# Performance work log

Measured on AMD Instinct MI355X. Metric: run time of the kernel, lower is better.

Reference implementation:

```python
import jax, jax.numpy as jnp
import numpy as np

SPARSITY = 0.1  # fraction k of weights kept (matches init sparsity)


def _subnet(scores, k):
    # Faithful to GetSubnet.forward: sort flattened scores ascending,
    # zero the bottom (1-k)*n entries, set the top k*n entries to 1.
    n = scores.size
    j = int((1.0 - k) * n)  # static under jit
    idx = jnp.argsort(scores.ravel())  # ascending, like torch .sort()
    flat = jnp.zeros((n,), scores.dtype).at[idx[j:]].set(1.0)
    return flat.reshape(scores.shape)


def setup_inputs() -> dict:
    key = jax.random.key(0)
    k1, k2 = jax.random.split(key)
    down_mask = jax.random.normal(k1, (8192, 2048), dtype=jnp.float32)
    up_mask = jax.random.normal(k2, (2048, 8192), dtype=jnp.float32)
    return {"down_mask": down_mask, "up_mask": up_mask}


def reference(down_mask, up_mask):
    # AdapterSubnet.forward: binary top-k masks of |down_mask| and |up_mask|
    return (_subnet(jnp.abs(down_mask), SPARSITY),
            _subnet(jnp.abs(up_mask), SPARSITY))
```

## Files before the change

kernel.cpp:

```cpp
#include <hip/hip_runtime.h>

using u32 = unsigned int;

#define H1_BINS 4096
#define H2_BINS 2048
#define H3_BINS 256
#define H1_OFF  0
#define H2_OFF  (H1_OFF + 2 * H1_BINS)
#define H3_OFF  (H2_OFF + 2 * H2_BINS)
#define SEL_OFF (H3_OFF + 2 * H3_BINS)
#define SEL_WORDS 8
#define EQ_OFF  (SEL_OFF + 2 * SEL_WORDS)
#define EQ_CAP  4096
#define ZERO_WORDS EQ_OFF

__device__ __forceinline__ u32 absbits(u32 x) { return x & 0x7FFFFFFFu; }

__global__ void k_hist1(const float* __restrict__ in0, const float* __restrict__ in1,
                        int n0, int n1, u32* __restrict__ ws) {
    __shared__ u32 h[H1_BINS];
    const int m = blockIdx.y;
    const u32* in = (const u32*)(m ? in1 : in0);
    const int n = m ? n1 : n0;
    const int n4 = n >> 2;
    for (int i = threadIdx.x; i < H1_BINS; i += blockDim.x) h[i] = 0;
    __syncthreads();
    const uint4* v = (const uint4*)in;
    const int stride = gridDim.x * blockDim.x;
    for (int i = blockIdx.x * blockDim.x + threadIdx.x; i < n4; i += stride) {
        uint4 x = v[i];
        atomicAdd(&h[absbits(x.x) >> 19], 1u);
        atomicAdd(&h[absbits(x.y) >> 19], 1u);
        atomicAdd(&h[absbits(x.z) >> 19], 1u);
        atomicAdd(&h[absbits(x.w) >> 19], 1u);
    }
    if (blockIdx.x == 0 && (int)threadIdx.x < (n & 3)) {
        u32 u = absbits(in[n4 * 4 + threadIdx.x]);
        atomicAdd(&h[u >> 19], 1u);
    }
    __syncthreads();
    u32* g = ws + H1_OFF + m * H1_BINS;
    for (int i = threadIdx.x; i < H1_BINS; i += blockDim.x)
        if (h[i]) atomicAdd(&g[i], h[i]);
}

__global__ void k_hist2(const float* __restrict__ in0, const float* __restrict__ in1,
                        int n0, int n1, u32* __restrict__ ws) {
    __shared__ u32 h[H2_BINS];
    const int m = blockIdx.y;
    const u32* in = (const u32*)(m ? in1 : in0);
    const int n = m ? n1 : n0;
    const int n4 = n >> 2;
    const u32 p1 = ws[SEL_OFF + m * SEL_WORDS + 0];
    for (int i = threadIdx.x; i < H2_BINS; i += blockDim.x) h[i] = 0;
    __syncthreads();
    const uint4* v = (const uint4*)in;
    const int stride = gridDim.x * blockDim.x;
    for (int i = blockIdx.x * blockDim.x + threadIdx.x; i < n4; i += stride) {
        uint4 x = v[i];
        u32 a;
        a = absbits(x.x); if ((a >> 19) == p1) atomicAdd(&h[(a >> 8) & 0x7FFu], 1u);
        a = absbits(x.y); if ((a >> 19) == p1) atomicAdd(&h[(a >> 8) & 0x7FFu], 1u);
        a = absbits(x.z); if ((a >> 19) == p1) atomicAdd(&h[(a >> 8) & 0x7FFu], 1u);
        a = absbits(x.w); if ((a >> 19) == p1) atomicAdd(&h[(a >> 8) & 0x7FFu], 1u);
    }
    if (blockIdx.x == 0 && (int)threadIdx.x < (n & 3)) {
        u32 a = absbits(in[n4 * 4 + threadIdx.x]);
        if ((a >> 19) == p1) atomicAdd(&h[(a >> 8) & 0x7FFu], 1u);
    }
    __syncthreads();
    u32* g = ws + H2_OFF + m * H2_BINS;
    for (int i = threadIdx.x; i < H2_BINS; i += blockDim.x)
        if (h[i]) atomicAdd(&g[i], h[i]);
}

__global__ void k_hist3(const float* __restrict__ in0, const float* __restrict__ in1,
                        int n0, int n1, u32* __restrict__ ws) {
    __shared__ u32 h[H3_BINS];
    const int m = blockIdx.y;
    const u32* in = (const u32*)(m ? in1 : in0);
    const int n = m ? n1 : n0;
    const int n4 = n >> 2;
    const u32* sel = ws + SEL_OFF + m * SEL_WORDS;
    const u32 pre20 = (sel[0] << 11) | sel[1];
    for (int i = threadIdx.x; i < H3_BINS; i += blockDim.x) h[i] = 0;
    __syncthreads();
    const uint4* v = (const uint4*)in;
    const int stride = gridDim.x * blockDim.x;
    for (int i = blockIdx.x * blockDim.x + threadIdx.x; i < n4; i += stride) {
        uint4 x = v[i];
        u32 a;
        a = absbits(x.x); if ((a >> 8) == pre20) atomicAdd(&h[a & 0xFFu], 1u);
        a = absbits(x.y); if ((a >> 8) == pre20) atomicAdd(&h[a & 0xFFu], 1u);
        a = absbits(x.z); if ((a >> 8) == pre20) atomicAdd(&h[a & 0xFFu], 1u);
        a = absbits(x.w); if ((a >> 8) == pre20) atomicAdd(&h[a & 0xFFu], 1u);
    }
    if (blockIdx.x == 0 && (int)threadIdx.x < (n & 3)) {
        u32 a = absbits(in[n4 * 4 + threadIdx.x]);
        if ((a >> 8) == pre20) atomicAdd(&h[a & 0xFFu], 1u);
    }
    __syncthreads();
    u32* g = ws + H3_OFF + m * H3_BINS;
    for (int i = threadIdx.x; i < H3_BINS; i += blockDim.x)
        if (h[i]) atomicAdd(&g[i], h[i]);
}

__global__ void k_select(u32* __restrict__ ws, int pass, int K0, int K1) {
    __shared__ u32 sh[256];
    const int m = blockIdx.x;
    u32* sel = ws + SEL_OFF + m * SEL_WORDS;
    const u32* hist;
    int bins;
    if (pass == 0)      { hist = ws + H1_OFF + m * H1_BINS; bins = H1_BINS; }
    else if (pass == 1) { hist = ws + H2_OFF + m * H2_BINS; bins = H2_BINS; }
    else                { hist = ws + H3_OFF + m * H3_BINS; bins = H3_BINS; }
    const u32 K = (u32)(m ? K1 : K0);
    u32 Gprev = 0;
    if (pass == 1) Gprev = sel[2];
    else if (pass == 2) Gprev = sel[5];
    const u32 Krem = K - Gprev;

    const int tid = threadIdx.x;
    const int C = bins / 256;
    const int base = tid * C;
    u32 s = 0;
    for (int i = 0; i < C; i++) s += hist[base + i];
    sh[tid] = s;
    __syncthreads();
    if (tid == 0) {
        u32 run = 0;
        for (int i = 255; i >= 0; i--) { u32 x = sh[i]; sh[i] = run; run += x; }
    }
    __syncthreads();
    u32 running = sh[tid];
    for (int bin = base + C - 1; bin >= base; bin--) {
        u32 c = hist[bin];
        if (running < Krem && running + c >= Krem) {
            if (pass == 0)      { sel[0] = (u32)bin; sel[2] = running; }
            else if (pass == 1) { sel[1] = (u32)bin; sel[5] = Gprev + running; }
            else {
                sel[3] = (sel[0] << 19) | (sel[1] << 8) | (u32)bin;
                sel[4] = Krem - running;
            }
        }
        running += c;
    }
}

__global__ void k_mask(const float* __restrict__ in0, const float* __restrict__ in1,
                       float* __restrict__ out0, float* __restrict__ out1,
                       int n0, int n1, u32* __restrict__ ws) {
    const int m = blockIdx.y;
    const u32* in = (const u32*)(m ? in1 : in0);
    float* out = m ? out1 : out0;
    const int n = m ? n1 : n0;
    const int n4 = n >> 2;
    u32* sel = ws + SEL_OFF + m * SEL_WORDS;
    const u32 t = sel[3];
    u32* eq = ws + EQ_OFF + m * EQ_CAP;
    const uint4* v = (const uint4*)in;
    float4* o = (float4*)out;
    const int stride = gridDim.x * blockDim.x;
    for (int i = blockIdx.x * blockDim.x + threadIdx.x; i < n4; i += stride) {
        uint4 x = v[i];
        u32 a0 = absbits(x.x), a1 = absbits(x.y), a2 = absbits(x.z), a3 = absbits(x.w);
        float4 r;
        r.x = (a0 > t) ? 1.0f : 0.0f;
        r.y = (a1 > t) ? 1.0f : 0.0f;
        r.z = (a2 > t) ? 1.0f : 0.0f;
        r.w = (a3 > t) ? 1.0f : 0.0f;
        o[i] = r;
        if (a0 == t) { u32 p = atomicAdd(&sel[6], 1u); if (p < EQ_CAP) eq[p] = (u32)(4 * i + 0); }
        if (a1 == t) { u32 p = atomicAdd(&sel[6], 1u); if (p < EQ_CAP) eq[p] = (u32)(4 * i + 1); }
        if (a2 == t) { u32 p = atomicAdd(&sel[6], 1u); if (p < EQ_CAP) eq[p] = (u32)(4 * i + 2); }
        if (a3 == t) { u32 p = atomicAdd(&sel[6], 1u); if (p < EQ_CAP) eq[p] = (u32)(4 * i + 3); }
    }
    if (blockIdx.x == 0 && (int)threadIdx.x < (n & 3)) {
        int idx = n4 * 4 + threadIdx.x;
        u32 a = absbits(in[idx]);
        out[idx] = (a > t) ? 1.0f : 0.0f;
        if (a == t) { u32 p = atomicAdd(&sel[6], 1u); if (p < EQ_CAP) eq[p] = (u32)idx; }
    }
}

__global__ void k_tie(float* __restrict__ out0, float* __restrict__ out1, u32* __restrict__ ws) {
    const int m = blockIdx.x;
    float* out = m ? out1 : out0;
    u32* sel = ws + SEL_OFF + m * SEL_WORDS;
    u32 E = sel[6]; if (E > EQ_CAP) E = EQ_CAP;
    const u32 R = sel[4];
    const u32* eq = ws + EQ_OFF + m * EQ_CAP;
    for (u32 e = threadIdx.x; e < E; e += blockDim.x) {
        u32 idx = eq[e];
        u32 cnt = 0;
        for (u32 e2 = 0; e2 < E; e2++) cnt += (eq[e2] > idx) ? 1u : 0u;
        if (cnt < R) out[idx] = 1.0f;
    }
}

extern "C" void kernel_launch(void* const* d_in, const int* in_sizes, int n_in,
                              void* d_out, int out_size, void* d_ws, size_t ws_size,
                              hipStream_t stream) {
    const float* in0 = (const float*)d_in[0];
    const float* in1 = (const float*)d_in[1];
    const int n0 = in_sizes[0];
    const int n1 = in_sizes[1];
    float* out0 = (float*)d_out;
    float* out1 = out0 + n0;
    u32* ws = (u32*)d_ws;

    const double k = 0.1;
    const int j0 = (int)((1.0 - k) * (double)n0);
    const int j1 = (int)((1.0 - k) * (double)n1);
    const int K0 = n0 - j0;
    const int K1 = n1 - j1;

    hipMemsetAsync(ws, 0, ZERO_WORDS * sizeof(u32), stream);

    dim3 hgrid(1024, 2);
    k_hist1<<<hgrid, 256, 0, stream>>>(in0, in1, n0, n1, ws);
    k_select<<<2, 256, 0, stream>>>(ws, 0, K0, K1);
    k_hist2<<<hgrid, 256, 0, stream>>>(in0, in1, n0, n1, ws);
    k_select<<<2, 256, 0, stream>>>(ws, 1, K0, K1);
    k_hist3<<<hgrid, 256, 0, stream>>>(in0, in1, n0, n1, ws);
    k_select<<<2, 256, 0, stream>>>(ws, 2, K0, K1);
    k_mask<<<dim3(1024, 2), 256, 0, stream>>>(in0, in1, out0, out1, n0, n1, ws);
    k_tie<<<2, 256, 0, stream>>>(out0, out1, ws);
}
```

Measured before the change: 335.0 us.

## Compact boundary-bucket candidates and fold select into last-block histogram kernels

```diff
diff --git a/kernel.cpp b/kernel.cpp
--- a/kernel.cpp
+++ b/kernel.cpp
@@ -1,6 +1,7 @@
 #include <hip/hip_runtime.h>
 
 using u32 = unsigned int;
+using u64 = unsigned long long;
 
 #define H1_BINS 4096
 #define H2_BINS 2048
@@ -9,155 +10,129 @@
 #define H2_OFF  (H1_OFF + 2 * H1_BINS)
 #define H3_OFF  (H2_OFF + 2 * H2_BINS)
 #define SEL_OFF (H3_OFF + 2 * H3_BINS)
-#define SEL_WORDS 8
-#define EQ_OFF  (SEL_OFF + 2 * SEL_WORDS)
-#define EQ_CAP  4096
-#define ZERO_WORDS EQ_OFF
+#define SEL_WORDS 16
+#define CTR_OFF  (SEL_OFF + 2 * SEL_WORDS)
+#define GCNT_OFF (CTR_OFF + 8)
+#define ECNT_OFF (GCNT_OFF + 2)
+#define ZERO_WORDS (ECNT_OFF + 2)
+#define EQ_OFF   12848
+#define EQ_CAP   4096
+#define CAND_OFF (EQ_OFF + 2 * EQ_CAP)
+#define GCAP     (1u << 21)
+#define SCAP     2048
 
 __device__ __forceinline__ u32 absbits(u32 x) { return x & 0x7FFFFFFFu; }
+__device__ __forceinline__ u32 aload(u32* p)  { return atomicAdd(p, 0u); }
+
+template<int BINS>
+__device__ void block_select(u32* hist, u32 Krem, u32* selBin, u32* selAbove) {
+    __shared__ u32 sh[256];
+    constexpr int C = BINS / 256;
+    u32 loc[C];
+    const int tid = threadIdx.x;
+    const int base = tid * C;
+    u32 s = 0;
+    for (int i = 0; i < C; i++) { loc[i] = aload(&hist[base + i]); s += loc[i]; }
+    sh[tid] = s;
+    __syncthreads();
+    if (tid == 0) {
+        u32 run = 0;
+        for (int i = 255; i >= 0; i--) { u32 x = sh[i]; sh[i] = run; run += x; }
+    }
+    __syncthreads();
+    u32 running = sh[tid];
+    for (int b = C - 1; b >= 0; b--) {
+        u32 c = loc[b];
+        if (running < Krem && running + c >= Krem) { *selBin = (u32)(base + b); *selAbove = running; }
+        running += c;
+    }
+}
 
 __global__ void k_hist1(const float* __restrict__ in0, const float* __restrict__ in1,
-                        int n0, int n1, u32* __restrict__ ws) {
-    __shared__ u32 h[H1_BINS];
+                        int n0, int n1, u32* __restrict__ ws, int K0, int K1) {
     const int m = blockIdx.y;
     const u32* in = (const u32*)(m ? in1 : in0);
     const int n = m ? n1 : n0;
     const int n4 = n >> 2;
-    for (int i = threadIdx.x; i < H1_BINS; i += blockDim.x) h[i] = 0;
-    __syncthreads();
+    u32* g = ws + H1_OFF + m * H1_BINS;
+    __shared__ u32 h[2][H1_BINS];
+    for (int i = threadIdx.x; i < H1_BINS; i += blockDim.x) { h[0][i] = 0; h[1][i] = 0; }
+    __syncthreads();
+    u32* hp = h[threadIdx.x >> 7];
     const uint4* v = (const uint4*)in;
     const int stride = gridDim.x * blockDim.x;
     for (int i = blockIdx.x * blockDim.x + threadIdx.x; i < n4; i += stride) {
         uint4 x = v[i];
-        atomicAdd(&h[absbits(x.x) >> 19], 1u);
-        atomicAdd(&h[absbits(x.y) >> 19], 1u);
-        atomicAdd(&h[absbits(x.z) >> 19], 1u);
-        atomicAdd(&h[absbits(x.w) >> 19], 1u);
-    }
-    if (blockIdx.x == 0 && (int)threadIdx.x < (n & 3)) {
-        u32 u = absbits(in[n4 * 4 + threadIdx.x]);
-        atomicAdd(&h[u >> 19], 1u);
-    }
-    __syncthreads();
-    u32* g = ws + H1_OFF + m * H1_BINS;
-    for (int i = threadIdx.x; i < H1_BINS; i += blockDim.x)
-        if (h[i]) atomicAdd(&g[i], h[i]);
-}
-
-__global__ void k_hist2(const float* __restrict__ in0, const float* __restrict__ in1,
-                        int n0, int n1, u32* __restrict__ ws) {
-    __shared__ u32 h[H2_BINS];
-    const int m = blockIdx.y;
-    const u32* in = (const u32*)(m ? in1 : in0);
-    const int n = m ? n1 : n0;
-    const int n4 = n >> 2;
-    const u32 p1 = ws[SEL_OFF + m * SEL_WORDS + 0];
-    for (int i = threadIdx.x; i < H2_BINS; i += blockDim.x) h[i] = 0;
-    __syncthreads();
-    const uint4* v = (const uint4*)in;
-    const int stride = gridDim.x * blockDim.x;
-    for (int i = blockIdx.x * blockDim.x + threadIdx.x; i < n4; i += stride) {
-        uint4 x = v[i];
-        u32 a;
-        a = absbits(x.x); if ((a >> 19) == p1) atomicAdd(&h[(a >> 8) & 0x7FFu], 1u);
-        a = absbits(x.y); if ((a >> 19) == p1) atomicAdd(&h[(a >> 8) & 0x7FFu], 1u);
-        a = absbits(x.z); if ((a >> 19) == p1) atomicAdd(&h[(a >> 8) & 0x7FFu], 1u);
-        a = absbits(x.w); if ((a >> 19) == p1) atomicAdd(&h[(a >> 8) & 0x7FFu], 1u);
-    }
-    if (blockIdx.x == 0 && (int)threadIdx.x < (n & 3)) {
-        u32 a = absbits(in[n4 * 4 + threadIdx.x]);
-        if ((a >> 19) == p1) atomicAdd(&h[(a >> 8) & 0x7FFu], 1u);
-    }
-    __syncthreads();
-    u32* g = ws + H2_OFF + m * H2_BINS;
-    for (int i = threadIdx.x; i < H2_BINS; i += blockDim.x)
-        if (h[i]) atomicAdd(&g[i], h[i]);
-}
-
-__global__ void k_hist3(const float* __restrict__ in0, const float* __restrict__ in1,
-                        int n0, int n1, u32* __restrict__ ws) {
-    __shared__ u32 h[H3_BINS];
-    const int m = blockIdx.y;
-    const u32* in = (const u32*)(m ? in1 : in0);
-    const int n = m ? n1 : n0;
-    const int n4 = n >> 2;
-    const u32* sel = ws + SEL_OFF + m * SEL_WORDS;
-    const u32 pre20 = (sel[0] << 11) | sel[1];
-    for (int i = threadIdx.x; i < H3_BINS; i += blockDim.x) h[i] = 0;
-    __syncthreads();
-    const uint4* v = (const uint4*)in;
-    const int stride = gridDim.x * blockDim.x;
-    for (int i = blockIdx.x * blockDim.x + threadIdx.x; i < n4; i += stride) {
-        uint4 x = v[i];
-        u32 a;
-        a = absbits(x.x); if ((a >> 8) == pre20) atomicAdd(&h[a & 0xFFu], 1u);
-        a = absbits(x.y); if ((a >> 8) == pre20) atomicAdd(&h[a & 0xFFu], 1u);
-        a = absbits(x.z); if ((a >> 8) == pre20) atomicAdd(&h[a & 0xFFu], 1u);
-        a = absbits(x.w); if ((a >> 8) == pre20) atomicAdd(&h[a & 0xFFu], 1u);
-    }
-    if (blockIdx.x == 0 && (int)threadIdx.x < (n & 3)) {
-        u32 a = absbits(in[n4 * 4 + threadIdx.x]);
-        if ((a >> 8) == pre20) atomicAdd(&h[a & 0xFFu], 1u);
-    }
-    __syncthreads();
-    u32* g = ws + H3_OFF + m * H3_BINS;
-    for (int i = threadIdx.x; i < H3_BINS; i += blockDim.x)
-        if (h[i]) atomicAdd(&g[i], h[i]);
-}
-
-__global__ void k_select(u32* __restrict__ ws, int pass, int K0, int K1) {
-    __shared__ u32 sh[256];
-    const int m = blockIdx.x;
-    u32* sel = ws + SEL_OFF + m * SEL_WORDS;
-    const u32* hist;
-    int bins;
-    if (pass == 0)      { hist = ws + H1_OFF + m * H1_BINS; bins = H1_BINS; }
-    else if (pass == 1) { hist = ws + H2_OFF + m * H2_BINS; bins = H2_BINS; }
-    else                { hist = ws + H3_OFF + m * H3_BINS; bins = H3_BINS; }
-    const u32 K = (u32)(m ? K1 : K0);
-    u32 Gprev = 0;
-    if (pass == 1) Gprev = sel[2];
-    else if (pass == 2) Gprev = sel[5];
-    const u32 Krem = K - Gprev;
-
-    const int tid = threadIdx.x;
-    const int C = bins / 256;
-    const int base = tid * C;
-    u32 s = 0;
-    for (int i = 0; i < C; i++) s += hist[base + i];
-    sh[tid] = s;
-    __syncthreads();
-    if (tid == 0) {
-        u32 run = 0;
-        for (int i = 255; i >= 0; i--) { u32 x = sh[i]; sh[i] = run; run += x; }
-    }
-    __syncthreads();
-    u32 running = sh[tid];
-    for (int bin = base + C - 1; bin >= base; bin--) {
-        u32 c = hist[bin];
-        if (running < Krem && running + c >= Krem) {
-            if (pass == 0)      { sel[0] = (u32)bin; sel[2] = running; }
-            else if (pass == 1) { sel[1] = (u32)bin; sel[5] = Gprev + running; }
-            else {
-                sel[3] = (sel[0] << 19) | (sel[1] << 8) | (u32)bin;
-                sel[4] = Krem - running;
-            }
-        }
-        running += c;
-    }
-}
-
-__global__ void k_mask(const float* __restrict__ in0, const float* __restrict__ in1,
-                       float* __restrict__ out0, float* __restrict__ out1,
-                       int n0, int n1, u32* __restrict__ ws) {
+        atomicAdd(&hp[absbits(x.x) >> 19], 1u);
+        atomicAdd(&hp[absbits(x.y) >> 19], 1u);
+        atomicAdd(&hp[absbits(x.z) >> 19], 1u);
+        atomicAdd(&hp[absbits(x.w) >> 19], 1u);
+    }
+    if (blockIdx.x == 0 && (int)threadIdx.x < (n & 3))
+        atomicAdd(&hp[absbits(in[n4 * 4 + threadIdx.x]) >> 19], 1u);
+    __syncthreads();
+    for (int i = threadIdx.x; i < H1_BINS; i += blockDim.x) {
+        u32 t = h[0][i] + h[1][i];
+        if (t) atomicAdd(&g[i], t);
+    }
+    __syncthreads();
+    __shared__ bool last;
+    if (threadIdx.x == 0) {
+        __threadfence();
+        last = (atomicAdd(&ws[CTR_OFF + m], 1u) == gridDim.x - 1);
+    }
+    __syncthreads();
+    if (last) {
+        __shared__ u32 tb, ta;
+        const u32 K = (u32)(m ? K1 : K0);
+        block_select<H1_BINS>(g, K, &tb, &ta);
+        __syncthreads();
+        if (threadIdx.x == 0) {
+            u32* sel = ws + SEL_OFF + m * SEL_WORDS;
+            sel[0] = tb;
+            sel[2] = ta;
+        }
+    }
+}
+
+__global__ void k_mask_compact(const float* __restrict__ in0, const float* __restrict__ in1,
+                               float* __restrict__ out0, float* __restrict__ out1,
+                               int n0, int n1, u32* __restrict__ ws) {
     const int m = blockIdx.y;
     const u32* in = (const u32*)(m ? in1 : in0);
     float* out = m ? out1 : out0;
     const int n = m ? n1 : n0;
     const int n4 = n >> 2;
-    u32* sel = ws + SEL_OFF + m * SEL_WORDS;
-    const u32 t = sel[3];
-    u32* eq = ws + EQ_OFF + m * EQ_CAP;
+    const u32 p1 = ws[SEL_OFF + m * SEL_WORDS + 0];
+    u32* gcnt = &ws[GCNT_OFF + m];
+    uint2* cand = (uint2*)(ws + CAND_OFF) + (size_t)m * GCAP;
+
+    __shared__ u32 scnt;
+    __shared__ u32 gbase;
+    __shared__ uint2 stage[SCAP];
+    if (threadIdx.x == 0) scnt = 0;
+    __syncthreads();
+
+    const u32 lane = threadIdx.x & 63u;
+    const u64 lmask = (1ull << lane) - 1ull;
+
+    auto handle = [&](u32 a, u32 idx) {
+        bool pred = ((a >> 19) == p1);
+        u64 mk = __ballot(pred);
+        if (mk) {
+            u32 cnt = (u32)__popcll(mk);
+            int leader = __ffsll((unsigned long long)mk) - 1;
+            u32 base = 0;
+            if ((int)lane == leader) base = atomicAdd(&scnt, cnt);
+            base = __shfl(base, leader);
+            if (pred) {
+                u32 pos = base + (u32)__popcll(mk & lmask);
+                if (pos < SCAP) stage[pos] = make_uint2(a, idx);
+                else { u32 gp = atomicAdd(gcnt, 1u); if (gp < GCAP) cand[gp] = make_uint2(a, idx); }
+            }
+        }
+    };
+
     const uint4* v = (const uint4*)in;
     float4* o = (float4*)out;
     const int stride = gridDim.x * blockDim.x;
@@ -165,36 +140,144 @@
         uint4 x = v[i];
         u32 a0 = absbits(x.x), a1 = absbits(x.y), a2 = absbits(x.z), a3 = absbits(x.w);
         float4 r;
-        r.x = (a0 > t) ? 1.0f : 0.0f;
-        r.y = (a1 > t) ? 1.0f : 0.0f;
-        r.z = (a2 > t) ? 1.0f : 0.0f;
-        r.w = (a3 > t) ? 1.0f : 0.0f;
+        r.x = ((a0 >> 19) > p1) ? 1.0f : 0.0f;
+        r.y = ((a1 >> 19) > p1) ? 1.0f : 0.0f;
+        r.z = ((a2 >> 19) > p1) ? 1.0f : 0.0f;
+        r.w = ((a3 >> 19) > p1) ? 1.0f : 0.0f;
         o[i] = r;
-        if (a0 == t) { u32 p = atomicAdd(&sel[6], 1u); if (p < EQ_CAP) eq[p] = (u32)(4 * i + 0); }
-        if (a1 == t) { u32 p = atomicAdd(&sel[6], 1u); if (p < EQ_CAP) eq[p] = (u32)(4 * i + 1); }
-        if (a2 == t) { u32 p = atomicAdd(&sel[6], 1u); if (p < EQ_CAP) eq[p] = (u32)(4 * i + 2); }
-        if (a3 == t) { u32 p = atomicAdd(&sel[6], 1u); if (p < EQ_CAP) eq[p] = (u32)(4 * i + 3); }
+        handle(a0, (u32)(4 * i + 0));
+        handle(a1, (u32)(4 * i + 1));
+        handle(a2, (u32)(4 * i + 2));
+        handle(a3, (u32)(4 * i + 3));
     }
     if (blockIdx.x == 0 && (int)threadIdx.x < (n & 3)) {
         int idx = n4 * 4 + threadIdx.x;
         u32 a = absbits(in[idx]);
-        out[idx] = (a > t) ? 1.0f : 0.0f;
-        if (a == t) { u32 p = atomicAdd(&sel[6], 1u); if (p < EQ_CAP) eq[p] = (u32)idx; }
-    }
-}
-
-__global__ void k_tie(float* __restrict__ out0, float* __restrict__ out1, u32* __restrict__ ws) {
-    const int m = blockIdx.x;
+        out[idx] = ((a >> 19) > p1) ? 1.0f : 0.0f;
+        handle(a, (u32)idx);
+    }
+    __syncthreads();
+    if (threadIdx.x == 0) {
+        u32 c = scnt < SCAP ? scnt : SCAP;
+        gbase = atomicAdd(gcnt, c);
+    }
+    __syncthreads();
+    u32 c = scnt < SCAP ? scnt : SCAP;
+    for (u32 j = threadIdx.x; j < c; j += blockDim.x) {
+        u32 p = gbase + j;
+        if (p < GCAP) cand[p] = stage[j];
+    }
+}
+
+__global__ void k_cand_hist2(u32* __restrict__ ws, int K0, int K1) {
+    const int m = blockIdx.y;
+    u32 cnt0 = ws[GCNT_OFF + m];
+    const u32 cnt = cnt0 < GCAP ? cnt0 : GCAP;
+    const uint2* cand = (const uint2*)(ws + CAND_OFF) + (size_t)m * GCAP;
+    u32* g = ws + H2_OFF + m * H2_BINS;
+    __shared__ u32 h[H2_BINS];
+    for (int i = threadIdx.x; i < H2_BINS; i += blockDim.x) h[i] = 0;
+    __syncthreads();
+    const u32 stride = gridDim.x * blockDim.x;
+    for (u32 i = blockIdx.x * blockDim.x + threadIdx.x; i < cnt; i += stride)
+        atomicAdd(&h[(cand[i].x >> 8) & 0x7FFu], 1u);
+    __syncthreads();
+    for (int i = threadIdx.x; i < H2_BINS; i += blockDim.x)
+        if (h[i]) atomicAdd(&g[i], h[i]);
+    __syncthreads();
+    __shared__ bool last;
+    if (threadIdx.x == 0) {
+        __threadfence();
+        last = (atomicAdd(&ws[CTR_OFF + 2 + m], 1u) == gridDim.x - 1);
+    }
+    __syncthreads();
+    if (last) {
+        u32* sel = ws + SEL_OFF + m * SEL_WORDS;
+        const u32 K = (u32)(m ? K1 : K0);
+        const u32 G1 = sel[2];
+        __shared__ u32 tb, ta;
+        block_select<H2_BINS>(g, K - G1, &tb, &ta);
+        __syncthreads();
+        if (threadIdx.x == 0) { sel[1] = tb; sel[5] = G1 + ta; }
+    }
+}
+
+__global__ void k_cand_hist3(u32* __restrict__ ws, int K0, int K1) {
+    const int m = blockIdx.y;
+    u32 cnt0 = ws[GCNT_OFF + m];
+    const u32 cnt = cnt0 < GCAP ? cnt0 : GCAP;
+    const uint2* cand = (const uint2*)(ws + CAND_OFF) + (size_t)m * GCAP;
+    u32* sel = ws + SEL_OFF + m * SEL_WORDS;
+    const u32 p1 = sel[0], p2 = sel[1];
+    const u32 pre20 = (p1 << 11) | p2;
+    u32* g = ws + H3_OFF + m * H3_BINS;
+    __shared__ u32 h[H3_BINS];
+    for (int i = threadIdx.x; i < H3_BINS; i += blockDim.x) h[i] = 0;
+    __syncthreads();
+    const u32 stride = gridDim.x * blockDim.x;
+    for (u32 i = blockIdx.x * blockDim.x + threadIdx.x; i < cnt; i += stride) {
+        u32 a = cand[i].x;
+        if ((a >> 8) == pre20) atomicAdd(&h[a & 0xFFu], 1u);
+    }
+    __syncthreads();
+    for (int i = threadIdx.x; i < H3_BINS; i += blockDim.x)
+        if (h[i]) atomicAdd(&g[i], h[i]);
+    __syncthreads();
+    __shared__ bool last;
+    if (threadIdx.x == 0) {
+        __threadfence();
+        last = (atomicAdd(&ws[CTR_OFF + 4 + m], 1u) == gridDim.x - 1);
+    }
+    __syncthreads();
+    if (last) {
+        const u32 K = (u32)(m ? K1 : K0);
+        const u32 Krem3 = K - sel[5];
+        __shared__ u32 tb, ta;
+        block_select<H3_BINS>(g, Krem3, &tb, &ta);
+        __syncthreads();
+        if (threadIdx.x == 0) {
+            sel[3] = (p1 << 19) | (p2 << 8) | tb;
+            sel[4] = Krem3 - ta;
+        }
+    }
+}
+
+__global__ void k_final(float* __restrict__ out0, float* __restrict__ out1, u32* __restrict__ ws) {
+    const int m = blockIdx.y;
     float* out = m ? out1 : out0;
+    u32 cnt0 = ws[GCNT_OFF + m];
+    const u32 cnt = cnt0 < GCAP ? cnt0 : GCAP;
+    const uint2* cand = (const uint2*)(ws + CAND_OFF) + (size_t)m * GCAP;
     u32* sel = ws + SEL_OFF + m * SEL_WORDS;
-    u32 E = sel[6]; if (E > EQ_CAP) E = EQ_CAP;
-    const u32 R = sel[4];
-    const u32* eq = ws + EQ_OFF + m * EQ_CAP;
-    for (u32 e = threadIdx.x; e < E; e += blockDim.x) {
-        u32 idx = eq[e];
-        u32 cnt = 0;
-        for (u32 e2 = 0; e2 < E; e2++) cnt += (eq[e2] > idx) ? 1u : 0u;
-        if (cnt < R) out[idx] = 1.0f;
+    const u32 t = sel[3];
+    const u32 stride = gridDim.x * blockDim.x;
+    for (u32 i = blockIdx.x * blockDim.x + threadIdx.x; i < cnt; i += stride) {
+        uint2 cv = cand[i];
+        if (cv.x > t) out[cv.y] = 1.0f;
+        else if (cv.x == t) {
+            u32 e = atomicAdd(&ws[ECNT_OFF + m], 1u);
+            if (e < EQ_CAP) atomicExch(&ws[EQ_OFF + m * EQ_CAP + e], cv.y);
+        }
+    }
+    __shared__ bool last;
+    if (threadIdx.x == 0) {
+        __threadfence();
+        last = (atomicAdd(&ws[CTR_OFF + 6 + m], 1u) == gridDim.x - 1);
+    }
+    __syncthreads();
+    if (last) {
+        u32 E0 = aload(&ws[ECNT_OFF + m]);
+        u32 E = E0 < EQ_CAP ? E0 : EQ_CAP;
+        const u32 R = sel[4];
+        __shared__ u32 eqs[EQ_CAP];
+        for (u32 e = threadIdx.x; e < E; e += blockDim.x) eqs[e] = aload(&ws[EQ_OFF + m * EQ_CAP + e]);
+        __syncthreads();
+        for (u32 e = threadIdx.x; e < E; e += blockDim.x) {
+            u32 idx = eqs[e];
+            u32 c = 0;
+            for (u32 e2 = 0; e2 < E; e2++) c += (eqs[e2] > idx) ? 1u : 0u;
+            if (c < R) out[idx] = 1.0f;
+        }
     }
 }
 
@@ -210,20 +293,13 @@
     u32* ws = (u32*)d_ws;
 
     const double k = 0.1;
-    const int j0 = (int)((1.0 - k) * (double)n0);
-    const int j1 = (int)((1.0 - k) * (double)n1);
-    const int K0 = n0 - j0;
-    const int K1 = n1 - j1;
+    const int K0 = n0 - (int)((1.0 - k) * (double)n0);
+    const int K1 = n1 - (int)((1.0 - k) * (double)n1);
 
     hipMemsetAsync(ws, 0, ZERO_WORDS * sizeof(u32), stream);
-
-    dim3 hgrid(1024, 2);
-    k_hist1<<<hgrid, 256, 0, stream>>>(in0, in1, n0, n1, ws);
-    k_select<<<2, 256, 0, stream>>>(ws, 0, K0, K1);
-    k_hist2<<<hgrid, 256, 0, stream>>>(in0, in1, n0, n1, ws);
-    k_select<<<2, 256, 0, stream>>>(ws, 1, K0, K1);
-    k_hist3<<<hgrid, 256, 0, stream>>>(in0, in1, n0, n1, ws);
-    k_select<<<2, 256, 0, stream>>>(ws, 2, K0, K1);
-    k_mask<<<dim3(1024, 2), 256, 0, stream>>>(in0, in1, out0, out1, n0, n1, ws);
-    k_tie<<<2, 256, 0, stream>>>(out0, out1, ws);
-}
+    k_hist1<<<dim3(1024, 2), 256, 0, stream>>>(in0, in1, n0, n1, ws, K0, K1);
+    k_mask_compact<<<dim3(1024, 2), 256, 0, stream>>>(in0, in1, out0, out1, n0, n1, ws);
+    k_cand_hist2<<<dim3(64, 2), 256, 0, stream>>>(ws, K0, K1);
+    k_cand_hist3<<<dim3(64, 2), 256, 0, stream>>>(ws, K0, K1);
+    k_final<<<dim3(64, 2), 256, 0, stream>>>(out0, out1, ws);
+}
```

New measurement: 374.2 us. 11.7% more time.
